# Kernel optimization log

Hardware: AMD Instinct MI355X
Metric: run time of the kernel (lower is better)

Reference implementation:

```python
import jax, jax.numpy as jnp
import numpy as np

NEG_SLOPE = 0.2
EPS = 1e-16


def gat_conv(x, edge_index, W, a_src, a_dst, b, heads, out_c, concat):
    # PyG GATConv: lin (no bias) -> per-head attention logits -> self-loops ->
    # leaky_relu -> softmax over incoming edges per dst -> weighted scatter-add -> bias
    N = x.shape[0]
    loop = jnp.arange(N)
    src = jnp.concatenate([edge_index[0], loop])  # [E+N]
    dst = jnp.concatenate([edge_index[1], loop])
    h = (x @ W).reshape(N, heads, out_c)                    # [N,H,C]
    a_s = jnp.sum(h * a_src[None], axis=-1)                 # [N,H]
    a_d = jnp.sum(h * a_dst[None], axis=-1)                 # [N,H]
    e = jax.nn.leaky_relu(a_s[src] + a_d[dst], NEG_SLOPE)   # [E+N,H]
    m = jax.ops.segment_max(e, dst, num_segments=N)         # stable softmax per dst
    e = jnp.exp(e - m[dst])
    s = jax.ops.segment_sum(e, dst, num_segments=N)
    alpha = e / (s[dst] + EPS)                              # [E+N,H]
    msg = h[src] * alpha[:, :, None]                        # [E+N,H,C]
    out = jax.ops.segment_sum(msg, dst, num_segments=N)     # [N,H,C]
    out = out.reshape(N, heads * out_c) if concat else out.mean(axis=1)
    return out + b


def setup_inputs() -> dict:
    key = jax.random.key(0)
    ks = jax.random.split(key, 20)
    N, E = 50000, 800000
    IN, HID, H, OUT = 128, 32, 4, 1
    HC = H * HID  # 128
    g = lambda k, shp: jax.random.normal(k, shp, dtype=jnp.float32) * 0.05
    inp = {
        "x": jax.random.normal(ks[0], (N, IN), dtype=jnp.float32),
        "edge_index": jax.random.randint(ks[1], (2, E), 0, N, dtype=jnp.int64),
        "batch": jnp.zeros((N,), dtype=jnp.int64),
        # conv0: GATConv(128 -> 32, heads=4, concat)
        "c0_w": g(ks[2], (IN, HC)), "c0_asrc": g(ks[3], (H, HID)),
        "c0_adst": g(ks[4], (H, HID)), "c0_b": jnp.zeros((HC,), jnp.float32),
        "s0_w": g(ks[5], (HC, IN)), "s0_b": jnp.zeros((HC,), jnp.float32),
        # conv1: GATConv(128 -> 32, heads=4, concat)
        "c1_w": g(ks[6], (HC, HC)), "c1_asrc": g(ks[7], (H, HID)),
        "c1_adst": g(ks[8], (H, HID)), "c1_b": jnp.zeros((HC,), jnp.float32),
        "s1_w": g(ks[9], (HC, HC)), "s1_b": jnp.zeros((HC,), jnp.float32),
        # conv2: GATConv(128 -> 1, heads=1, concat=False)
        "c2_w": g(ks[10], (HC, OUT)), "c2_asrc": g(ks[11], (1, OUT)),
        "c2_adst": g(ks[12], (1, OUT)), "c2_b": jnp.zeros((OUT,), jnp.float32),
        "s2_w": g(ks[13], (OUT, HC)), "s2_b": jnp.zeros((OUT,), jnp.float32),
    }
    return inp


def reference(x, edge_index, batch,
              c0_w, c0_asrc, c0_adst, c0_b, s0_w, s0_b,
              c1_w, c1_asrc, c1_adst, c1_b, s1_w, s1_b,
              c2_w, c2_asrc, c2_adst, c2_b, s2_w, s2_b):
    # layer 0 (dropout is identity in eval mode)
    h = jax.nn.relu(gat_conv(x, edge_index, c0_w, c0_asrc, c0_adst, c0_b, 4, 32, True)
                    + x @ s0_w.T + s0_b)
    # layer 1
    h = jax.nn.relu(gat_conv(h, edge_index, c1_w, c1_asrc, c1_adst, c1_b, 4, 32, True)
                    + h @ s1_w.T + s1_b)
    # output layer: heads=1, concat=False (mean over heads)
    h = (gat_conv(h, edge_index, c2_w, c2_asrc, c2_adst, c2_b, 1, 1, False)
         + h @ s2_w.T + s2_b)
    return jax.nn.sigmoid(h)
```

## Files before the change

### kernel.cpp

```cpp
#include <hip/hip_runtime.h>
#include <math.h>

#define TPB 256
#define RB 128

typedef short bf16x8 __attribute__((ext_vector_type(8)));
typedef float f32x4 __attribute__((ext_vector_type(4)));

static __device__ __forceinline__ float lrelu(float x) { return x > 0.f ? x : 0.2f * x; }
static __device__ __forceinline__ unsigned short f2bf(float f) {
  unsigned u = __float_as_uint(f);
  u += 0x7fffu + ((u >> 16) & 1u);
  return (unsigned short)(u >> 16);
}
static __device__ __forceinline__ float bflo(unsigned w) { return __uint_as_float(w << 16); }
static __device__ __forceinline__ float bfhi(unsigned w) { return __uint_as_float(w & 0xffff0000u); }
static __device__ __forceinline__ bf16x8 pack8(float4 v0, float4 v1) {
  bf16x8 r;
  r[0] = (short)f2bf(v0.x);
  r[1] = (short)f2bf(v0.y);
  r[2] = (short)f2bf(v0.z);
  r[3] = (short)f2bf(v0.w);
  r[4] = (short)f2bf(v1.x);
  r[5] = (short)f2bf(v1.y);
  r[6] = (short)f2bf(v1.z);
  r[7] = (short)f2bf(v1.w);
  return r;
}

__global__ void k_hist8(const int* __restrict__ dstE, int E, int N, int* __restrict__ deg) {
  int r = blockIdx.x & 7;
  int nb = gridDim.x >> 3;
  int lo = (int)(((long)r * N) / 8), hi = (int)(((long)(r + 1) * N) / 8);
  int EN = E + N;
  for (int e = (blockIdx.x >> 3) * TPB + threadIdx.x; e < EN; e += nb * TPB) {
    int d = (e < E) ? dstE[e] : (e - E);
    d = min(max(d, 0), N - 1);
    if (d >= lo && d < hi) atomicAdd(&deg[d], 1);
  }
}

__global__ void k_scan1(const int* __restrict__ deg, int N, int* __restrict__ csum) {
  __shared__ int sm[TPB];
  int t = threadIdx.x, i = blockIdx.x * TPB + t;
  sm[t] = (i < N) ? deg[i] : 0;
  __syncthreads();
  for (int off = TPB / 2; off; off >>= 1) {
    if (t < off) sm[t] += sm[t + off];
    __syncthreads();
  }
  if (t == 0) csum[blockIdx.x] = sm[0];
}

__global__ void k_scan2(int* __restrict__ csum, int nch) {
  __shared__ int sm[TPB];
  int t = threadIdx.x;
  int v = (t < nch) ? csum[t] : 0;
  sm[t] = v;
  __syncthreads();
  for (int off = 1; off < TPB; off <<= 1) {
    int add = (t >= off) ? sm[t - off] : 0;
    __syncthreads();
    sm[t] += add;
    __syncthreads();
  }
  if (t < nch) csum[t] = (t == 0) ? 0 : sm[t - 1];
}

__global__ void k_scan3(const int* __restrict__ deg, const int* __restrict__ csum, int N, int total,
                        int* __restrict__ row_ptr, int* __restrict__ cursor) {
  __shared__ int sm[TPB];
  int b = blockIdx.x, t = threadIdx.x, i = b * TPB + t;
  int v = (i < N) ? deg[i] : 0;
  sm[t] = v;
  __syncthreads();
  for (int off = 1; off < TPB; off <<= 1) {
    int add = (t >= off) ? sm[t - off] : 0;
    __syncthreads();
    sm[t] += add;
    __syncthreads();
  }
  if (i < N) {
    int rp = csum[b] + sm[t] - v;
    row_ptr[i] = rp;
    cursor[i] = rp;
  }
  if (i == 0) row_ptr[N] = total;
}

__global__ void k_scatter8(const int* __restrict__ srcE, const int* __restrict__ dstE, int E, int N,
                           int* __restrict__ cursor, int* __restrict__ csr_src) {
  int r = blockIdx.x & 7;
  int nb = gridDim.x >> 3;
  int lo = (int)(((long)r * N) / 8), hi = (int)(((long)(r + 1) * N) / 8);
  int EN = E + N;
  for (int e = (blockIdx.x >> 3) * TPB + threadIdx.x; e < EN; e += nb * TPB) {
    int d = (e < E) ? dstE[e] : (e - E);
    d = min(max(d, 0), N - 1);
    if (d >= lo && d < hi) {
      int s = (e < E) ? srcE[e] : (e - E);
      s = min(max(s, 0), N - 1);
      int pos = atomicAdd(&cursor[d], 1);
      csr_src[pos] = s;
    }
  }
}

__global__ void k_prep_w2(const float* __restrict__ cW0, const float* __restrict__ sW0,
                          const float* __restrict__ cW1, const float* __restrict__ sW1,
                          unsigned short* __restrict__ Wb0, unsigned short* __restrict__ Wb1) {
  int j = blockIdx.x & 255;
  int which = blockIdx.x >> 8;
  int k = threadIdx.x;
  const float* cW = which ? cW1 : cW0;
  const float* sW = which ? sW1 : sW0;
  unsigned short* Wb = which ? Wb1 : Wb0;
  Wb[j * 128 + k] = f2bf((j < 128) ? cW[k * 128 + j] : sW[(j - 128) * 128 + k]);
}

template <bool F32IN>
__global__ __launch_bounds__(TPB) void k_gemm_mfma(const void* __restrict__ Xv,
                                                   const unsigned short* __restrict__ Wb,
                                                   unsigned short* __restrict__ H16,
                                                   unsigned short* __restrict__ Sk16, int NR) {
  int wid = threadIdx.x >> 6, lane = threadIdx.x & 63;
  int r0 = blockIdx.x * 64;
  int c0 = wid * 64;
  int l15 = lane & 15, lk = lane >> 4;

  f32x4 acc[4][4];
#pragma unroll
  for (int i = 0; i < 4; ++i)
#pragma unroll
    for (int j = 0; j < 4; ++j) acc[i][j] = (f32x4){0.f, 0.f, 0.f, 0.f};

#pragma unroll
  for (int ks = 0; ks < 4; ++ks) {
    bf16x8 a[4], b[4];
#pragma unroll
    for (int rt = 0; rt < 4; ++rt) {
      int row = min(r0 + rt * 16 + l15, NR - 1);
      if (F32IN) {
        const float* xp = (const float*)Xv + (size_t)row * 128 + ks * 32 + lk * 8;
        a[rt] = pack8(*(const float4*)xp, *(const float4*)(xp + 4));
      } else {
        a[rt] = *(const bf16x8*)((const unsigned short*)Xv + (size_t)row * 128 + ks * 32 + lk * 8);
      }
    }
#pragma unroll
    for (int ct = 0; ct < 4; ++ct) {
      int col = c0 + ct * 16 + l15;
      b[ct] = *(const bf16x8*)(Wb + (size_t)col * 128 + ks * 32 + lk * 8);
    }
#pragma unroll
    for (int rt = 0; rt < 4; ++rt)
#pragma unroll
      for (int ct = 0; ct < 4; ++ct)
        acc[rt][ct] = __builtin_amdgcn_mfma_f32_16x16x32_bf16(a[rt], b[ct], acc[rt][ct], 0, 0, 0);
  }

  int orow = lk * 4;
#pragma unroll
  for (int rt = 0; rt < 4; ++rt) {
#pragma unroll
    for (int ct = 0; ct < 4; ++ct) {
      int col = c0 + ct * 16 + l15;
#pragma unroll
      for (int r = 0; r < 4; ++r) {
        int row = r0 + rt * 16 + orow + r;
        if (row < NR) {
          float v = acc[rt][ct][r];
          if (col < 128)
            H16[(size_t)row * 128 + col] = f2bf(v);
          else
            Sk16[(size_t)row * 128 + (col - 128)] = f2bf(v);
        }
      }
    }
  }
}

__global__ void k_asad(const unsigned short* __restrict__ H16, const float* __restrict__ asrc,
                       const float* __restrict__ adst, float* __restrict__ a_s, float* __restrict__ a_d, int N) {
  int i = blockIdx.x * TPB + threadIdx.x;
  if (i >= N * 4) return;
  int n = i >> 2, h = i & 3;
  const uint4* hp = (const uint4*)(H16 + (size_t)n * 128 + h * 32);
  const float4* ap = (const float4*)(asrc + h * 32);
  const float4* bp = (const float4*)(adst + h * 32);
  float sa = 0.f, sd = 0.f;
#pragma unroll
  for (int q = 0; q < 4; ++q) {
    uint4 v = hp[q];
    float f0 = bflo(v.x), f1 = bfhi(v.x), f2 = bflo(v.y), f3 = bfhi(v.y);
    float f4 = bflo(v.z), f5 = bfhi(v.z), f6 = bflo(v.w), f7 = bfhi(v.w);
    float4 a0 = ap[q * 2], a1 = ap[q * 2 + 1];
    float4 b0 = bp[q * 2], b1 = bp[q * 2 + 1];
    sa += f0 * a0.x + f1 * a0.y + f2 * a0.z + f3 * a0.w + f4 * a1.x + f5 * a1.y + f6 * a1.z + f7 * a1.w;
    sd += f0 * b0.x + f1 * b0.y + f2 * b0.z + f3 * b0.w + f4 * b1.x + f5 * b1.y + f6 * b1.z + f7 * b1.w;
  }
  a_s[i] = sa;
  a_d[i] = sd;
}

template <bool BF, bool L2F>
__global__ __launch_bounds__(TPB) void k_smax_agg(
    const int* __restrict__ row_ptr, const int* __restrict__ csr_src, const float4* __restrict__ a_s4,
    const float4* __restrict__ a_d4, const unsigned short* __restrict__ H16,
    const unsigned short* __restrict__ Sk16, const float* __restrict__ cb, const float* __restrict__ sb,
    float4* __restrict__ spill, unsigned short* __restrict__ XnB, const float* __restrict__ c2w,
    const float* __restrict__ s2w, const float* __restrict__ c2as, const float* __restrict__ c2ad,
    float* __restrict__ h2, float* __restrict__ sk2, float* __restrict__ as2, float* __restrict__ ad2, int N) {
  __shared__ int s_src[4][64];
  __shared__ float s_al[4][64][4];
  int wid = threadIdx.x >> 6;
  int n = blockIdx.x * 4 + wid;
  if (n >= N) return;
  int lane = threadIdx.x & 63;
  int eg = lane >> 4, cl = lane & 15;
  int h = cl >> 2;
  int beg = row_ptr[n], end = row_ptr[n + 1];
  int deg = end - beg;
  float4 ad = a_d4[n];
  float acc[8];
#pragma unroll
  for (int i = 0; i < 8; ++i) acc[i] = 0.f;

  if (deg <= 64) {
    int s_l = 0;
    float4 lg = make_float4(-1e30f, -1e30f, -1e30f, -1e30f);
    if (lane < deg) {
      s_l = csr_src[beg + lane];
      float4 as = a_s4[s_l];
      lg.x = lrelu(as.x + ad.x);
      lg.y = lrelu(as.y + ad.y);
      lg.z = lrelu(as.z + ad.z);
      lg.w = lrelu(as.w + ad.w);
    }
    int maxoff = (deg <= 16) ? 8 : (deg <= 32) ? 16 : 32;
    float4 mx = lg;
    for (int off = 1; off <= maxoff; off <<= 1) {
      mx.x = fmaxf(mx.x, __shfl_xor(mx.x, off));
      mx.y = fmaxf(mx.y, __shfl_xor(mx.y, off));
      mx.z = fmaxf(mx.z, __shfl_xor(mx.z, off));
      mx.w = fmaxf(mx.w, __shfl_xor(mx.w, off));
    }
    float4 pv = make_float4(0.f, 0.f, 0.f, 0.f);
    if (lane < deg) {
      pv.x = __expf(lg.x - mx.x);
      pv.y = __expf(lg.y - mx.y);
      pv.z = __expf(lg.z - mx.z);
      pv.w = __expf(lg.w - mx.w);
    }
    float4 sm = pv;
    for (int off = 1; off <= maxoff; off <<= 1) {
      sm.x += __shfl_xor(sm.x, off);
      sm.y += __shfl_xor(sm.y, off);
      sm.z += __shfl_xor(sm.z, off);
      sm.w += __shfl_xor(sm.w, off);
    }
    pv.x *= 1.f / (sm.x + 1e-16f);
    pv.y *= 1.f / (sm.y + 1e-16f);
    pv.z *= 1.f / (sm.z + 1e-16f);
    pv.w *= 1.f / (sm.w + 1e-16f);
    s_src[wid][lane] = s_l;
    *(float4*)&s_al[wid][lane][0] = pv;
    __builtin_amdgcn_wave_barrier();

    int dpad = (deg + 3) & ~3;
    for (int j = 0; j < dpad; j += 4) {
      int sj = s_src[wid][j + eg];
      float aj = s_al[wid][j + eg][h];
      uint4 w = *(const uint4*)(H16 + (size_t)sj * 128 + cl * 8);
      acc[0] = fmaf(aj, bflo(w.x), acc[0]);
      acc[1] = fmaf(aj, bfhi(w.x), acc[1]);
      acc[2] = fmaf(aj, bflo(w.y), acc[2]);
      acc[3] = fmaf(aj, bfhi(w.y), acc[3]);
      acc[4] = fmaf(aj, bflo(w.z), acc[4]);
      acc[5] = fmaf(aj, bfhi(w.z), acc[5]);
      acc[6] = fmaf(aj, bflo(w.w), acc[6]);
      acc[7] = fmaf(aj, bfhi(w.w), acc[7]);
    }
  } else {
    float4 mx = make_float4(-1e30f, -1e30f, -1e30f, -1e30f);
    for (int p = beg + lane; p < end; p += 64) {
      int s = csr_src[p];
      float4 as = a_s4[s];
      float4 lg;
      lg.x = lrelu(as.x + ad.x);
      lg.y = lrelu(as.y + ad.y);
      lg.z = lrelu(as.z + ad.z);
      lg.w = lrelu(as.w + ad.w);
      spill[p] = lg;
      mx.x = fmaxf(mx.x, lg.x);
      mx.y = fmaxf(mx.y, lg.y);
      mx.z = fmaxf(mx.z, lg.z);
      mx.w = fmaxf(mx.w, lg.w);
    }
#pragma unroll
    for (int off = 32; off; off >>= 1) {
      mx.x = fmaxf(mx.x, __shfl_xor(mx.x, off));
      mx.y = fmaxf(mx.y, __shfl_xor(mx.y, off));
      mx.z = fmaxf(mx.z, __shfl_xor(mx.z, off));
      mx.w = fmaxf(mx.w, __shfl_xor(mx.w, off));
    }
    __threadfence_block();
    float4 sm = make_float4(0.f, 0.f, 0.f, 0.f);
    for (int p = beg + lane; p < end; p += 64) {
      float4 lg = spill[p];
      float4 pv;
      pv.x = __expf(lg.x - mx.x);
      pv.y = __expf(lg.y - mx.y);
      pv.z = __expf(lg.z - mx.z);
      pv.w = __expf(lg.w - mx.w);
      spill[p] = pv;
      sm.x += pv.x;
      sm.y += pv.y;
      sm.z += pv.z;
      sm.w += pv.w;
    }
#pragma unroll
    for (int off = 32; off; off >>= 1) {
      sm.x += __shfl_xor(sm.x, off);
      sm.y += __shfl_xor(sm.y, off);
      sm.z += __shfl_xor(sm.z, off);
      sm.w += __shfl_xor(sm.w, off);
    }
    float invh = 1.f / (((h == 0) ? sm.x : (h == 1) ? sm.y : (h == 2) ? sm.z : sm.w) + 1e-16f);
    __threadfence_block();
    const float* af = (const float*)spill;
    for (int p = beg + eg; p < end; p += 4) {
      int s = csr_src[p];
      float aj = af[(size_t)p * 4 + h] * invh;
      uint4 w = *(const uint4*)(H16 + (size_t)s * 128 + cl * 8);
      acc[0] = fmaf(aj, bflo(w.x), acc[0]);
      acc[1] = fmaf(aj, bfhi(w.x), acc[1]);
      acc[2] = fmaf(aj, bflo(w.y), acc[2]);
      acc[3] = fmaf(aj, bfhi(w.y), acc[3]);
      acc[4] = fmaf(aj, bflo(w.z), acc[4]);
      acc[5] = fmaf(aj, bfhi(w.z), acc[5]);
      acc[6] = fmaf(aj, bflo(w.w), acc[6]);
      acc[7] = fmaf(aj, bfhi(w.w), acc[7]);
    }
  }

#pragma unroll
  for (int i = 0; i < 8; ++i) {
    acc[i] += __shfl_xor(acc[i], 16);
    acc[i] += __shfl_xor(acc[i], 32);
  }

  int c = cl * 8;
  uint4 skw = *(const uint4*)(Sk16 + (size_t)n * 128 + c);
  float4 cb0 = *(const float4*)(cb + c), cb1 = *(const float4*)(cb + c + 4);
  float4 sb0 = *(const float4*)(sb + c), sb1 = *(const float4*)(sb + c + 4);
  float o[8];
  o[0] = fmaxf(acc[0] + cb0.x + bflo(skw.x) + sb0.x, 0.f);
  o[1] = fmaxf(acc[1] + cb0.y + bfhi(skw.x) + sb0.y, 0.f);
  o[2] = fmaxf(acc[2] + cb0.z + bflo(skw.y) + sb0.z, 0.f);
  o[3] = fmaxf(acc[3] + cb0.w + bfhi(skw.y) + sb0.w, 0.f);
  o[4] = fmaxf(acc[4] + cb1.x + bflo(skw.z) + sb1.x, 0.f);
  o[5] = fmaxf(acc[5] + cb1.y + bfhi(skw.z) + sb1.y, 0.f);
  o[6] = fmaxf(acc[6] + cb1.z + bflo(skw.w) + sb1.z, 0.f);
  o[7] = fmaxf(acc[7] + cb1.w + bfhi(skw.w) + sb1.w, 0.f);

  if (BF && eg == 0) {
    uint4 pk;
    pk.x = (unsigned)f2bf(o[0]) | ((unsigned)f2bf(o[1]) << 16);
    pk.y = (unsigned)f2bf(o[2]) | ((unsigned)f2bf(o[3]) << 16);
    pk.z = (unsigned)f2bf(o[4]) | ((unsigned)f2bf(o[5]) << 16);
    pk.w = (unsigned)f2bf(o[6]) | ((unsigned)f2bf(o[7]) << 16);
    *(uint4*)(XnB + (size_t)n * 128 + c) = pk;
  }
  if (L2F) {
    float4 w0 = *(const float4*)(c2w + c), w1 = *(const float4*)(c2w + c + 4);
    float4 v0 = *(const float4*)(s2w + c), v1 = *(const float4*)(s2w + c + 4);
    float dh = o[0] * w0.x + o[1] * w0.y + o[2] * w0.z + o[3] * w0.w + o[4] * w1.x + o[5] * w1.y + o[6] * w1.z +
               o[7] * w1.w;
    float ds = o[0] * v0.x + o[1] * v0.y + o[2] * v0.z + o[3] * v0.w + o[4] * v1.x + o[5] * v1.y + o[6] * v1.z +
               o[7] * v1.w;
#pragma unroll
    for (int off = 1; off <= 8; off <<= 1) {
      dh += __shfl_xor(dh, off);
      ds += __shfl_xor(ds, off);
    }
    if (lane == 0) {
      h2[n] = dh;
      sk2[n] = ds;
      as2[n] = dh * c2as[0];
      ad2[n] = dh * c2ad[0];
    }
  }
}

__global__ __launch_bounds__(TPB) void k_l2_smax_agg(const int* __restrict__ row_ptr, const int* __restrict__ csr_src,
                                                     const float* __restrict__ as2, const float* __restrict__ ad2,
                                                     const float* __restrict__ h2, const float* __restrict__ sk2,
                                                     const float* __restrict__ c2b, const float* __restrict__ s2b,
                                                     float* __restrict__ out, int N) {
  int n = blockIdx.x * 4 + (threadIdx.x >> 6);
  if (n >= N) return;
  int lane = threadIdx.x & 63;
  int beg = row_ptr[n], end = row_ptr[n + 1];
  int deg = end - beg;
  float ad = ad2[n];
  float num = 0.f, den = 0.f;

  if (deg <= 64) {
    float lg = -1e30f, hv = 0.f;
    if (lane < deg) {
      int s = csr_src[beg + lane];
      lg = lrelu(as2[s] + ad);
      hv = h2[s];
    }
    float mx = lg;
#pragma unroll
    for (int off = 32; off; off >>= 1) mx = fmaxf(mx, __shfl_xor(mx, off));
    float pv = (lane < deg) ? __expf(lg - mx) : 0.f;
    num = pv * hv;
    den = pv;
  } else {
    float mx = -1e30f;
    for (int p = beg + lane; p < end; p += 64) mx = fmaxf(mx, lrelu(as2[csr_src[p]] + ad));
#pragma unroll
    for (int off = 32; off; off >>= 1) mx = fmaxf(mx, __shfl_xor(mx, off));
    for (int p = beg + lane; p < end; p += 64) {
      int s = csr_src[p];
      float pv = __expf(lrelu(as2[s] + ad) - mx);
      num += pv * h2[s];
      den += pv;
    }
  }
#pragma unroll
  for (int off = 32; off; off >>= 1) {
    num += __shfl_xor(num, off);
    den += __shfl_xor(den, off);
  }
  if (lane == 0) {
    float v = num / (den + 1e-16f) + c2b[0] + sk2[n] + s2b[0];
    out[n] = 1.f / (1.f + __expf(-v));
  }
}

extern "C" void kernel_launch(void* const* d_in, const int* in_sizes, int n_in,
                              void* d_out, int out_size, void* d_ws, size_t ws_size,
                              hipStream_t stream) {
  const float* x = (const float*)d_in[0];
  const int* ei = (const int*)d_in[1];
  const float* c0_w = (const float*)d_in[3];
  const float* c0_as = (const float*)d_in[4];
  const float* c0_ad = (const float*)d_in[5];
  const float* c0_b = (const float*)d_in[6];
  const float* s0_w = (const float*)d_in[7];
  const float* s0_b = (const float*)d_in[8];
  const float* c1_w = (const float*)d_in[9];
  const float* c1_as = (const float*)d_in[10];
  const float* c1_ad = (const float*)d_in[11];
  const float* c1_b = (const float*)d_in[12];
  const float* s1_w = (const float*)d_in[13];
  const float* s1_b = (const float*)d_in[14];
  const float* c2_w = (const float*)d_in[15];
  const float* c2_as = (const float*)d_in[16];
  const float* c2_ad = (const float*)d_in[17];
  const float* c2_b = (const float*)d_in[18];
  const float* s2_w = (const float*)d_in[19];
  const float* s2_b = (const float*)d_in[20];

  const int N = in_sizes[0] / 128;
  const int E = in_sizes[1] / 2;
  const int EN = E + N;
  const int* srcE = ei;
  const int* dstE = ei + E;

  char* wp_ = (char*)d_ws;
  auto alloc = [&](size_t bytes) -> void* {
    void* r = (void*)wp_;
    wp_ += (bytes + 255) & ~(size_t)255;
    return r;
  };
  unsigned short* Xb1 = (unsigned short*)alloc((size_t)N * 128 * 2);
  unsigned short* H16 = (unsigned short*)alloc((size_t)N * 128 * 2);
  unsigned short* Sk16 = (unsigned short*)alloc((size_t)N * 128 * 2);
  float* a_s = (float*)alloc((size_t)N * 4 * 4);
  float* a_d = (float*)alloc((size_t)N * 4 * 4);
  float* spill = (float*)alloc((size_t)EN * 4 * 4);
  unsigned short* Wb0 = (unsigned short*)alloc(256 * 128 * 2);
  unsigned short* Wb1 = (unsigned short*)alloc(256 * 128 * 2);
  int* deg = (int*)alloc((size_t)N * 4);
  int* row_ptr = (int*)alloc((size_t)(N + 1) * 4);
  int* cursor = (int*)alloc((size_t)N * 4);
  int* csum = (int*)alloc(4096 * 4);
  int* csr_src = (int*)alloc((size_t)EN * 4);
  float* h2 = (float*)alloc((size_t)N * 4);
  float* sk2 = (float*)alloc((size_t)N * 4);
  float* as2 = (float*)alloc((size_t)N * 4);
  float* ad2 = (float*)alloc((size_t)N * 4);

  const int gN4 = (N * 4 + TPB - 1) / TPB;
  const int nch = (N + TPB - 1) / TPB;
  const int gGemm = (N + 63) / 64;
  const int gWave = (N + 3) / 4;

  hipMemsetAsync(deg, 0, (size_t)N * 4, stream);
  k_hist8<<<8 * RB, TPB, 0, stream>>>(dstE, E, N, deg);
  k_scan1<<<nch, TPB, 0, stream>>>(deg, N, csum);
  k_scan2<<<1, TPB, 0, stream>>>(csum, nch);
  k_scan3<<<nch, TPB, 0, stream>>>(deg, csum, N, EN, row_ptr, cursor);
  k_scatter8<<<8 * RB, TPB, 0, stream>>>(srcE, dstE, E, N, cursor, csr_src);

  k_prep_w2<<<512, 128, 0, stream>>>(c0_w, s0_w, c1_w, s1_w, Wb0, Wb1);

  k_gemm_mfma<true><<<gGemm, TPB, 0, stream>>>(x, Wb0, H16, Sk16, N);
  k_asad<<<gN4, TPB, 0, stream>>>(H16, c0_as, c0_ad, a_s, a_d, N);
  k_smax_agg<true, false><<<gWave, TPB, 0, stream>>>(row_ptr, csr_src, (const float4*)a_s, (const float4*)a_d,
                                                     H16, Sk16, c0_b, s0_b, (float4*)spill, Xb1, nullptr, nullptr,
                                                     nullptr, nullptr, nullptr, nullptr, nullptr, nullptr, N);

  k_gemm_mfma<false><<<gGemm, TPB, 0, stream>>>(Xb1, Wb1, H16, Sk16, N);
  k_asad<<<gN4, TPB, 0, stream>>>(H16, c1_as, c1_ad, a_s, a_d, N);
  k_smax_agg<false, true><<<gWave, TPB, 0, stream>>>(row_ptr, csr_src, (const float4*)a_s, (const float4*)a_d,
                                                     H16, Sk16, c1_b, s1_b, (float4*)spill, nullptr, c2_w, s2_w,
                                                     c2_as, c2_ad, h2, sk2, as2, ad2, N);

  k_l2_smax_agg<<<gWave, TPB, 0, stream>>>(row_ptr, csr_src, as2, ad2, h2, sk2, c2_b, s2_b, (float*)d_out, N);
}
```

Before: 374.2 us.

## Bucket edges by dst range, fold attention dots into GEMM, prefetch gathers

```diff
diff --git a/kernel.cpp b/kernel.cpp
--- a/kernel.cpp
+++ b/kernel.cpp
@@ -2,7 +2,6 @@
 #include <math.h>
 
 #define TPB 256
-#define RB 128
 
 typedef short bf16x8 __attribute__((ext_vector_type(8)));
 typedef float f32x4 __attribute__((ext_vector_type(4)));
@@ -28,16 +27,51 @@
   return r;
 }
 
-__global__ void k_hist8(const int* __restrict__ dstE, int E, int N, int* __restrict__ deg) {
+static __device__ __forceinline__ int range_of(int d, int N) {
+  int r = (int)(((long)d * 8) / N);
+  if (r > 7) r = 7;
+  while ((long)(r + 1) * N / 8 <= d) ++r;
+  while ((long)r * N / 8 > d) --r;
+  return r;
+}
+
+__global__ void k_bucket(const int* __restrict__ srcE, const int* __restrict__ dstE, int E, int N,
+                         int* __restrict__ bcur, unsigned* __restrict__ bucket, int BCAP) {
+  __shared__ int cnt[8];
+  __shared__ int base[8];
+  int t = threadIdx.x;
+  if (t < 8) cnt[t] = 0;
+  __syncthreads();
+  int e = blockIdx.x * TPB + t;
+  int EN = E + N;
+  int r = 0, loc = 0;
+  unsigned val = 0;
+  bool ok = (e < EN);
+  if (ok) {
+    int s = (e < E) ? srcE[e] : (e - E);
+    int d = (e < E) ? dstE[e] : (e - E);
+    s = min(max(s, 0), N - 1);
+    d = min(max(d, 0), N - 1);
+    r = range_of(d, N);
+    int lo = (int)(((long)r * N) / 8);
+    val = (unsigned)s | ((unsigned)(d - lo) << 16);
+    loc = atomicAdd(&cnt[r], 1);
+  }
+  __syncthreads();
+  if (t < 8) base[t] = atomicAdd(&bcur[t], cnt[t]);
+  __syncthreads();
+  if (ok) bucket[(size_t)r * BCAP + base[r] + loc] = val;
+}
+
+__global__ void k_hist_b(const unsigned* __restrict__ bucket, const int* __restrict__ bcur, int N,
+                         int* __restrict__ deg, int BCAP) {
   int r = blockIdx.x & 7;
   int nb = gridDim.x >> 3;
-  int lo = (int)(((long)r * N) / 8), hi = (int)(((long)(r + 1) * N) / 8);
-  int EN = E + N;
-  for (int e = (blockIdx.x >> 3) * TPB + threadIdx.x; e < EN; e += nb * TPB) {
-    int d = (e < E) ? dstE[e] : (e - E);
-    d = min(max(d, 0), N - 1);
-    if (d >= lo && d < hi) atomicAdd(&deg[d], 1);
-  }
+  int lo = (int)(((long)r * N) / 8);
+  int m = bcur[r];
+  const unsigned* b = bucket + (size_t)r * BCAP;
+  for (int i = (blockIdx.x >> 3) * TPB + threadIdx.x; i < m; i += nb * TPB)
+    atomicAdd(&deg[lo + (int)(b[i] >> 16)], 1);
 }
 
 __global__ void k_scan1(const int* __restrict__ deg, int N, int* __restrict__ csum) {
@@ -88,21 +122,17 @@
   if (i == 0) row_ptr[N] = total;
 }
 
-__global__ void k_scatter8(const int* __restrict__ srcE, const int* __restrict__ dstE, int E, int N,
-                           int* __restrict__ cursor, int* __restrict__ csr_src) {
+__global__ void k_scatter_b(const unsigned* __restrict__ bucket, const int* __restrict__ bcur, int N,
+                            int* __restrict__ cursor, int* __restrict__ csr_src, int BCAP) {
   int r = blockIdx.x & 7;
   int nb = gridDim.x >> 3;
-  int lo = (int)(((long)r * N) / 8), hi = (int)(((long)(r + 1) * N) / 8);
-  int EN = E + N;
-  for (int e = (blockIdx.x >> 3) * TPB + threadIdx.x; e < EN; e += nb * TPB) {
-    int d = (e < E) ? dstE[e] : (e - E);
-    d = min(max(d, 0), N - 1);
-    if (d >= lo && d < hi) {
-      int s = (e < E) ? srcE[e] : (e - E);
-      s = min(max(s, 0), N - 1);
-      int pos = atomicAdd(&cursor[d], 1);
-      csr_src[pos] = s;
-    }
+  int lo = (int)(((long)r * N) / 8);
+  int m = bcur[r];
+  const unsigned* b = bucket + (size_t)r * BCAP;
+  for (int i = (blockIdx.x >> 3) * TPB + threadIdx.x; i < m; i += nb * TPB) {
+    unsigned v = b[i];
+    int pos = atomicAdd(&cursor[lo + (int)(v >> 16)], 1);
+    csr_src[pos] = (int)(v & 0xFFFFu);
   }
 }
 
@@ -118,21 +148,48 @@
   Wb[j * 128 + k] = f2bf((j < 128) ? cW[k * 128 + j] : sW[(j - 128) * 128 + k]);
 }
 
+__global__ void k_prep_wx(const float* __restrict__ cW0, const float* __restrict__ as0,
+                          const float* __restrict__ ad0, const float* __restrict__ cW1,
+                          const float* __restrict__ as1, const float* __restrict__ ad1,
+                          unsigned short* __restrict__ Wx0, unsigned short* __restrict__ Wx1) {
+  int which = blockIdx.x;
+  const float* cW = which ? cW1 : cW0;
+  const float* asr = which ? as1 : as0;
+  const float* adr = which ? ad1 : ad0;
+  unsigned short* Wx = which ? Wx1 : Wx0;
+  int k = threadIdx.x;
+  for (int h = 0; h < 4; ++h) {
+    float sv = 0.f, su = 0.f;
+    for (int c = 0; c < 32; ++c) {
+      float w = cW[k * 128 + h * 32 + c];
+      sv += w * asr[h * 32 + c];
+      su += w * adr[h * 32 + c];
+    }
+    Wx[h * 128 + k] = f2bf(sv);
+    Wx[(4 + h) * 128 + k] = f2bf(su);
+  }
+}
+
 template <bool F32IN>
 __global__ __launch_bounds__(TPB) void k_gemm_mfma(const void* __restrict__ Xv,
                                                    const unsigned short* __restrict__ Wb,
+                                                   const unsigned short* __restrict__ Wx,
                                                    unsigned short* __restrict__ H16,
-                                                   unsigned short* __restrict__ Sk16, int NR) {
+                                                   unsigned short* __restrict__ Sk16, float* __restrict__ a_s,
+                                                   float* __restrict__ a_d, int NR) {
   int wid = threadIdx.x >> 6, lane = threadIdx.x & 63;
   int r0 = blockIdx.x * 64;
   int c0 = wid * 64;
   int l15 = lane & 15, lk = lane >> 4;
 
   f32x4 acc[4][4];
-#pragma unroll
-  for (int i = 0; i < 4; ++i)
+  f32x4 accx[4];
+#pragma unroll
+  for (int i = 0; i < 4; ++i) {
+    accx[i] = (f32x4){0.f, 0.f, 0.f, 0.f};
 #pragma unroll
     for (int j = 0; j < 4; ++j) acc[i][j] = (f32x4){0.f, 0.f, 0.f, 0.f};
+  }
 
 #pragma unroll
   for (int ks = 0; ks < 4; ++ks) {
@@ -157,6 +214,11 @@
 #pragma unroll
       for (int ct = 0; ct < 4; ++ct)
         acc[rt][ct] = __builtin_amdgcn_mfma_f32_16x16x32_bf16(a[rt], b[ct], acc[rt][ct], 0, 0, 0);
+    if (wid == 3) {
+      bf16x8 bx = *(const bf16x8*)(Wx + (size_t)l15 * 128 + ks * 32 + lk * 8);
+#pragma unroll
+      for (int rt = 0; rt < 4; ++rt) accx[rt] = __builtin_amdgcn_mfma_f32_16x16x32_bf16(a[rt], bx, accx[rt], 0, 0, 0);
+    }
   }
 
   int orow = lk * 4;
@@ -178,29 +240,22 @@
       }
     }
   }
-}
-
-__global__ void k_asad(const unsigned short* __restrict__ H16, const float* __restrict__ asrc,
-                       const float* __restrict__ adst, float* __restrict__ a_s, float* __restrict__ a_d, int N) {
-  int i = blockIdx.x * TPB + threadIdx.x;
-  if (i >= N * 4) return;
-  int n = i >> 2, h = i & 3;
-  const uint4* hp = (const uint4*)(H16 + (size_t)n * 128 + h * 32);
-  const float4* ap = (const float4*)(asrc + h * 32);
-  const float4* bp = (const float4*)(adst + h * 32);
-  float sa = 0.f, sd = 0.f;
-#pragma unroll
-  for (int q = 0; q < 4; ++q) {
-    uint4 v = hp[q];
-    float f0 = bflo(v.x), f1 = bfhi(v.x), f2 = bflo(v.y), f3 = bfhi(v.y);
-    float f4 = bflo(v.z), f5 = bfhi(v.z), f6 = bflo(v.w), f7 = bfhi(v.w);
-    float4 a0 = ap[q * 2], a1 = ap[q * 2 + 1];
-    float4 b0 = bp[q * 2], b1 = bp[q * 2 + 1];
-    sa += f0 * a0.x + f1 * a0.y + f2 * a0.z + f3 * a0.w + f4 * a1.x + f5 * a1.y + f6 * a1.z + f7 * a1.w;
-    sd += f0 * b0.x + f1 * b0.y + f2 * b0.z + f3 * b0.w + f4 * b1.x + f5 * b1.y + f6 * b1.z + f7 * b1.w;
-  }
-  a_s[i] = sa;
-  a_d[i] = sd;
+  if (wid == 3 && l15 < 8) {
+#pragma unroll
+    for (int rt = 0; rt < 4; ++rt) {
+#pragma unroll
+      for (int r = 0; r < 4; ++r) {
+        int row = r0 + rt * 16 + orow + r;
+        if (row < NR) {
+          float v = accx[rt][r];
+          if (l15 < 4)
+            a_s[(size_t)row * 4 + l15] = v;
+          else
+            a_d[(size_t)row * 4 + (l15 - 4)] = v;
+        }
+      }
+    }
+  }
 }
 
 template <bool BF, bool L2F>
@@ -268,18 +323,30 @@
     __builtin_amdgcn_wave_barrier();
 
     int dpad = (deg + 3) & ~3;
-    for (int j = 0; j < dpad; j += 4) {
-      int sj = s_src[wid][j + eg];
-      float aj = s_al[wid][j + eg][h];
+    if (dpad > 0) {
+      int sj = s_src[wid][eg];
+      float aj = s_al[wid][eg][h];
       uint4 w = *(const uint4*)(H16 + (size_t)sj * 128 + cl * 8);
-      acc[0] = fmaf(aj, bflo(w.x), acc[0]);
-      acc[1] = fmaf(aj, bfhi(w.x), acc[1]);
-      acc[2] = fmaf(aj, bflo(w.y), acc[2]);
-      acc[3] = fmaf(aj, bfhi(w.y), acc[3]);
-      acc[4] = fmaf(aj, bflo(w.z), acc[4]);
-      acc[5] = fmaf(aj, bfhi(w.z), acc[5]);
-      acc[6] = fmaf(aj, bflo(w.w), acc[6]);
-      acc[7] = fmaf(aj, bfhi(w.w), acc[7]);
+      for (int j = 0; j < dpad; j += 4) {
+        int jn = j + 4;
+        float ajn = 0.f;
+        uint4 wn = make_uint4(0, 0, 0, 0);
+        if (jn < dpad) {
+          int sjn = s_src[wid][jn + eg];
+          ajn = s_al[wid][jn + eg][h];
+          wn = *(const uint4*)(H16 + (size_t)sjn * 128 + cl * 8);
+        }
+        acc[0] = fmaf(aj, bflo(w.x), acc[0]);
+        acc[1] = fmaf(aj, bfhi(w.x), acc[1]);
+        acc[2] = fmaf(aj, bflo(w.y), acc[2]);
+        acc[3] = fmaf(aj, bfhi(w.y), acc[3]);
+        acc[4] = fmaf(aj, bflo(w.z), acc[4]);
+        acc[5] = fmaf(aj, bfhi(w.z), acc[5]);
+        acc[6] = fmaf(aj, bflo(w.w), acc[6]);
+        acc[7] = fmaf(aj, bfhi(w.w), acc[7]);
+        aj = ajn;
+        w = wn;
+      }
     }
   } else {
     float4 mx = make_float4(-1e30f, -1e30f, -1e30f, -1e30f);
@@ -471,6 +538,7 @@
   const int EN = E + N;
   const int* srcE = ei;
   const int* dstE = ei + E;
+  const int BCAP = EN;
 
   char* wp_ = (char*)d_ws;
   auto alloc = [&](size_t bytes) -> void* {
@@ -486,38 +554,43 @@
   float* spill = (float*)alloc((size_t)EN * 4 * 4);
   unsigned short* Wb0 = (unsigned short*)alloc(256 * 128 * 2);
   unsigned short* Wb1 = (unsigned short*)alloc(256 * 128 * 2);
+  unsigned short* Wx0 = (unsigned short*)alloc(16 * 128 * 2);
+  unsigned short* Wx1 = (unsigned short*)alloc(16 * 128 * 2);
+  int* bcur = (int*)alloc(64);
   int* deg = (int*)alloc((size_t)N * 4);
   int* row_ptr = (int*)alloc((size_t)(N + 1) * 4);
   int* cursor = (int*)alloc((size_t)N * 4);
   int* csum = (int*)alloc(4096 * 4);
   int* csr_src = (int*)alloc((size_t)EN * 4);
+  unsigned* bucket = (unsigned*)alloc((size_t)8 * BCAP * 4);
   float* h2 = (float*)alloc((size_t)N * 4);
   float* sk2 = (float*)alloc((size_t)N * 4);
   float* as2 = (float*)alloc((size_t)N * 4);
   float* ad2 = (float*)alloc((size_t)N * 4);
 
-  const int gN4 = (N * 4 + TPB - 1) / TPB;
   const int nch = (N + TPB - 1) / TPB;
   const int gGemm = (N + 63) / 64;
   const int gWave = (N + 3) / 4;
-
-  hipMemsetAsync(deg, 0, (size_t)N * 4, stream);
-  k_hist8<<<8 * RB, TPB, 0, stream>>>(dstE, E, N, deg);
+  const int gEN = (EN + TPB - 1) / TPB;
+  const int gRng = 8 * 64;
+
+  hipMemsetAsync(bcur, 0, 256 + (size_t)N * 4, stream);
+  k_bucket<<<gEN, TPB, 0, stream>>>(srcE, dstE, E, N, bcur, bucket, BCAP);
+  k_hist_b<<<gRng, TPB, 0, stream>>>(bucket, bcur, N, deg, BCAP);
   k_scan1<<<nch, TPB, 0, stream>>>(deg, N, csum);
   k_scan2<<<1, TPB, 0, stream>>>(csum, nch);
   k_scan3<<<nch, TPB, 0, stream>>>(deg, csum, N, EN, row_ptr, cursor);
-  k_scatter8<<<8 * RB, TPB, 0, stream>>>(srcE, dstE, E, N, cursor, csr_src);
+  k_scatter_b<<<gRng, TPB, 0, stream>>>(bucket, bcur, N, cursor, csr_src, BCAP);
 
   k_prep_w2<<<512, 128, 0, stream>>>(c0_w, s0_w, c1_w, s1_w, Wb0, Wb1);
-
-  k_gemm_mfma<true><<<gGemm, TPB, 0, stream>>>(x, Wb0, H16, Sk16, N);
-  k_asad<<<gN4, TPB, 0, stream>>>(H16, c0_as, c0_ad, a_s, a_d, N);
+  k_prep_wx<<<2, 128, 0, stream>>>(c0_w, c0_as, c0_ad, c1_w, c1_as, c1_ad, Wx0, Wx1);
+
+  k_gemm_mfma<true><<<gGemm, TPB, 0, stream>>>(x, Wb0, Wx0, H16, Sk16, a_s, a_d, N);
   k_smax_agg<true, false><<<gWave, TPB, 0, stream>>>(row_ptr, csr_src, (const float4*)a_s, (const float4*)a_d,
                                                      H16, Sk16, c0_b, s0_b, (float4*)spill, Xb1, nullptr, nullptr,
                                                      nullptr, nullptr, nullptr, nullptr, nullptr, nullptr, N);
 
-  k_gemm_mfma<false><<<gGemm, TPB, 0, stream>>>(Xb1, Wb1, H16, Sk16, N);
-  k_asad<<<gN4, TPB, 0, stream>>>(H16, c1_as, c1_ad, a_s, a_d, N);
+  k_gemm_mfma<false><<<gGemm, TPB, 0, stream>>>(Xb1, Wb1, Wx1, H16, Sk16, a_s, a_d, N);
   k_smax_agg<false, true><<<gWave, TPB, 0, stream>>>(row_ptr, csr_src, (const float4*)a_s, (const float4*)a_d,
                                                      H16, Sk16, c1_b, s1_b, (float4*)spill, nullptr, c2_w, s2_w,
                                                      c2_as, c2_ad, h2, sk2, as2, ad2, N);
```

Result: slower. 403.2 us (+7.7%).
